# Performance work log

Hardware: AMD Instinct MI355X
Metric: run time of the kernel (lower is better)

Reference implementation:

```python
import jax, jax.numpy as jnp
import numpy as np

N = 50000
E = 800000
H = 4
C = 64
IN = 61
NEG_SLOPE = 0.2


def setup_inputs() -> dict:
    key = jax.random.key(0)
    ks = jax.random.split(key, 20)
    x = jax.random.normal(ks[0], (N, IN), dtype=jnp.float32)
    edge_index = jax.random.randint(ks[1], (2, E), 0, N, dtype=jnp.int64)

    def glorot(k, shape):
        fan = shape[0] + shape[-1] if len(shape) == 2 else shape[-1] * 2
        s = jnp.sqrt(6.0 / fan)
        return jax.random.uniform(k, shape, jnp.float32, -s, s)

    dims = [IN, H * C, H * C]
    params = {}
    for i, din in enumerate(dims):
        params[f'w{i}'] = glorot(ks[2 + 4 * i], (din, H * C))
        params[f'att_src{i}'] = glorot(ks[3 + 4 * i], (H, C))
        params[f'att_dst{i}'] = glorot(ks[4 + 4 * i], (H, C))
        params[f'b{i}'] = jnp.zeros((H * C,), jnp.float32)
    params['head_w1'] = glorot(ks[14], (H * C, C))
    params['head_b1'] = jnp.zeros((C,), jnp.float32)
    params['head_w2'] = glorot(ks[15], (C, 1))
    params['head_b2'] = jnp.zeros((1,), jnp.float32)
    return dict(x=x, edge_index=edge_index, **params)


def _gat_layer(x, W, att_src, att_dst, bias, src, dst):
    # Linear transform -> [N, H, C]
    h = (x @ W).reshape(N, H, C)
    # Per-node attention logits
    a_src = jnp.einsum('nhc,hc->nh', h, att_src)  # [N, H]
    a_dst = jnp.einsum('nhc,hc->nh', h, att_dst)
    # Per-edge score, leaky relu
    e = jax.nn.leaky_relu(a_src[src] + a_dst[dst], NEG_SLOPE)  # [Etot, H]
    # Segment softmax over incoming edges of each dst node
    m = jax.ops.segment_max(e, dst, num_segments=N)  # [N, H]
    ex = jnp.exp(e - m[dst])
    denom = jax.ops.segment_sum(ex, dst, num_segments=N)
    alpha = ex / denom[dst]  # [Etot, H]
    # Scatter-aggregate messages
    out = jax.ops.segment_sum(h[src] * alpha[:, :, None], dst, num_segments=N)  # [N, H, C]
    return out.reshape(N, H * C) + bias


def reference(x, edge_index, w0, att_src0, att_dst0, b0,
              w1, att_src1, att_dst1, b1,
              w2, att_src2, att_dst2, b2,
              head_w1, head_b1, head_w2, head_b2):
    # PyG GATConv adds self-loops by default
    loop = jnp.arange(N, dtype=edge_index.dtype)
    src = jnp.concatenate([edge_index[0], loop])
    dst = jnp.concatenate([edge_index[1], loop])

    layers = [(w0, att_src0, att_dst0, b0),
              (w1, att_src1, att_dst1, b1),
              (w2, att_src2, att_dst2, b2)]
    h = x
    for (W, a_s, a_d, b) in layers:
        h = _gat_layer(h, W, a_s, a_d, b, src, dst)
        h = jax.nn.elu(h)  # dropout is identity in eval mode
    # MLP head
    h = jax.nn.relu(h @ head_w1 + head_b1)
    out = (h @ head_w2 + head_b2).squeeze(-1)  # [N]
    return out
```

## Files before the change

kernel.cpp:

```cpp
#include <hip/hip_runtime.h>
#include <cstdint>
#include <cstddef>

#define NN   50000
#define EE   800000
#define ETOT (EE + NN)
#define HC   256
#define NEG_SLOPE 0.2f
#define SENT_WORDS 25000
#define SENT_VAL 0x42C80000u

typedef __attribute__((ext_vector_type(8))) short g4_bf16x8;
typedef __attribute__((ext_vector_type(4))) float g4_f32x4;

__device__ __forceinline__ float g4_bf2f(unsigned short h) {
    union { unsigned int u; float f; } v;
    v.u = ((unsigned int)h) << 16;
    return v.f;
}
__device__ __forceinline__ unsigned short g4_f2bf(float f) {
    union { float f; unsigned int u; } v;
    v.f = f;
    unsigned int u = v.u;
    u += 0x7fffu + ((u >> 16) & 1u);
    return (unsigned short)(u >> 16);
}
__device__ __forceinline__ float g4_ld(const void* p, size_t i, int isf) {
    return isf ? ((const float*)p)[i] : g4_bf2f(((const unsigned short*)p)[i]);
}

__global__ void g4_detect(const unsigned int* __restrict__ xw,
                          const int* __restrict__ ei32, int* __restrict__ flags) {
    __shared__ int cnt[256];
    int t = threadIdx.x;
    unsigned int w = xw[t];
    int e = (int)((w >> 23) & 0xffu);
    cnt[t] = (e >= 110 && e <= 135) ? 1 : 0;
    __syncthreads();
    for (int off = 128; off > 0; off >>= 1) {
        if (t < off) cnt[t] += cnt[t + off];
        __syncthreads();
    }
    if (t == 0) {
        flags[0] = (cnt[0] >= 128) ? 1 : 0;
        int i64 = (ei32[1] == 0 && ei32[3] == 0 && ei32[5] == 0 &&
                   ei32[7] == 0 && ei32[9] == 0) ? 1 : 0;
        flags[1] = i64;
    }
}

__global__ void g4_zero(int* __restrict__ deg, int* __restrict__ cnt,
                        unsigned int* __restrict__ outw) {
    int i = blockIdx.x * 256 + threadIdx.x;
    if (i < NN) { deg[i] = 0; cnt[i] = 0; }
    if (i < SENT_WORDS) outw[i] = SENT_VAL;
}

__global__ void g4_hist(const int* __restrict__ ei, const int* __restrict__ flags,
                        int* __restrict__ deg) {
    int e = blockIdx.x * blockDim.x + threadIdx.x;
    if (e >= ETOT) return;
    int i64 = flags[1];
    int d;
    if (e < EE) d = i64 ? ei[2 * (EE + e)] : ei[EE + e];
    else        d = e - EE;
    atomicAdd(&deg[d], 1);
}

__global__ void g4_scan_block(const int* __restrict__ deg, int* __restrict__ tmp,
                              int* __restrict__ partial) {
    __shared__ int sh[256];
    int i = blockIdx.x * 256 + threadIdx.x;
    int v = (i < NN) ? deg[i] : 0;
    sh[threadIdx.x] = v;
    __syncthreads();
    for (int off = 1; off < 256; off <<= 1) {
        int t = (threadIdx.x >= off) ? sh[threadIdx.x - off] : 0;
        __syncthreads();
        sh[threadIdx.x] += t;
        __syncthreads();
    }
    if (i < NN) tmp[i] = sh[threadIdx.x] - v;
    if (threadIdx.x == 255) partial[blockIdx.x] = sh[255];
}

__global__ void g4_scan_partial(int* __restrict__ partial, int nb,
                                int* __restrict__ rowptrN) {
    __shared__ int sh[256];
    int v = (threadIdx.x < nb) ? partial[threadIdx.x] : 0;
    sh[threadIdx.x] = v;
    __syncthreads();
    for (int off = 1; off < 256; off <<= 1) {
        int t = (threadIdx.x >= off) ? sh[threadIdx.x - off] : 0;
        __syncthreads();
        sh[threadIdx.x] += t;
        __syncthreads();
    }
    if (threadIdx.x < nb) partial[threadIdx.x] = sh[threadIdx.x] - v;
    if (threadIdx.x == 0) *rowptrN = ETOT;
}

__global__ void g4_scan_add(const int* __restrict__ tmp, const int* __restrict__ partial,
                            int* __restrict__ rowptr) {
    int i = blockIdx.x * 256 + threadIdx.x;
    if (i < NN) rowptr[i] = tmp[i] + partial[blockIdx.x];
}

__global__ void g4_fill_csr(const int* __restrict__ ei, const int* __restrict__ flags,
                            const int* __restrict__ rowptr,
                            int* __restrict__ cnt, int* __restrict__ col) {
    int e = blockIdx.x * blockDim.x + threadIdx.x;
    if (e >= ETOT) return;
    int i64 = flags[1];
    int s, d;
    if (e < EE) {
        s = i64 ? ei[2 * e] : ei[e];
        d = i64 ? ei[2 * (EE + e)] : ei[EE + e];
    } else {
        s = e - EE; d = e - EE;
    }
    int pos = rowptr[d] + atomicAdd(&cnt[d], 1);
    col[pos] = s;
}

__global__ void g4_bprep(const void* __restrict__ B, const int* __restrict__ flags,
                         unsigned short* __restrict__ Bt, int K, int kshift, int Nc) {
    int i = blockIdx.x * 256 + threadIdx.x;
    int KP = 1 << kshift;
    if (i >= Nc << kshift) return;
    int n = i >> kshift;
    int k = i & (KP - 1);
    unsigned short v = 0;
    if (k < K) {
        if (flags[0]) v = g4_f2bf(((const float*)B)[(size_t)k * Nc + n]);
        else          v = ((const unsigned short*)B)[(size_t)k * Nc + n];
    }
    Bt[(size_t)n * KP + k] = v;
}

#define LDK 40
__global__ __launch_bounds__(256) void g4_gemm2(
    const void* __restrict__ A, int a_mode, const unsigned short* __restrict__ Bt,
    const int* __restrict__ flags, unsigned short* __restrict__ C,
    const void* __restrict__ att_src, const void* __restrict__ att_dst,
    float* __restrict__ a_srcO, float* __restrict__ a_dstO,
    int M, int K, int KP) {
    __shared__ short As[64 * LDK];
    __shared__ short Bs[256 * LDK];
    const int isf = flags[0];
    const int af  = (a_mode == 0) ? isf : 0;
    const int tid  = threadIdx.x;
    const int lane = tid & 63;
    const int wc   = tid >> 6;
    const int quad = lane >> 4;
    const int l15  = lane & 15;
    const int bm = blockIdx.x * 64;
    const int a_vec = (af == 0) && ((K & 31) == 0);

    g4_f32x4 acc[4][4];
    #pragma unroll
    for (int it = 0; it < 4; it++)
        #pragma unroll
        for (int jt = 0; jt < 4; jt++) {
            acc[it][jt].x = 0.f; acc[it][jt].y = 0.f;
            acc[it][jt].z = 0.f; acc[it][jt].w = 0.f;
        }

    for (int k0 = 0; k0 < KP; k0 += 32) {
        {
            int row = tid >> 2, kc = (tid & 3) * 8;
            int gm = bm + row;
            short v[8];
            if (a_vec && gm < M) {
                *(g4_bf16x8*)v = *(const g4_bf16x8*)((const short*)A + (size_t)gm * K + k0 + kc);
            } else {
                #pragma unroll
                for (int j = 0; j < 8; j++) {
                    int gk = k0 + kc + j;
                    if (gm < M && gk < K) {
                        if (af == 0) v[j] = ((const short*)A)[(size_t)gm * K + gk];
                        else         v[j] = (short)g4_f2bf(((const float*)A)[(size_t)gm * K + gk]);
                    } else v[j] = 0;
                }
            }
            *(g4_bf16x8*)&As[row * LDK + kc] = *(g4_bf16x8*)v;
        }
        {
            const unsigned short* bp = Bt + (size_t)tid * KP + k0;
            short* dst = &Bs[tid * LDK];
            *(g4_bf16x8*)(dst + 0)  = *(const g4_bf16x8*)(bp + 0);
            *(g4_bf16x8*)(dst + 8)  = *(const g4_bf16x8*)(bp + 8);
            *(g4_bf16x8*)(dst + 16) = *(const g4_bf16x8*)(bp + 16);
            *(g4_bf16x8*)(dst + 24) = *(const g4_bf16x8*)(bp + 24);
        }
        __syncthreads();
        g4_bf16x8 afr[4], bfr[4];
        #pragma unroll
        for (int it = 0; it < 4; it++)
            afr[it] = *(const g4_bf16x8*)&As[(it * 16 + l15) * LDK + quad * 8];
        #pragma unroll
        for (int jt = 0; jt < 4; jt++)
            bfr[jt] = *(const g4_bf16x8*)&Bs[(wc * 64 + jt * 16 + l15) * LDK + quad * 8];
        #pragma unroll
        for (int it = 0; it < 4; it++)
            #pragma unroll
            for (int jt = 0; jt < 4; jt++)
                acc[it][jt] = __builtin_amdgcn_mfma_f32_16x16x32_bf16(
                    afr[it], bfr[jt], acc[it][jt], 0, 0, 0);
        __syncthreads();
    }
    #pragma unroll
    for (int it = 0; it < 4; it++) {
        #pragma unroll
        for (int jt = 0; jt < 4; jt++) {
            int gn   = wc * 64 + jt * 16 + l15;
            int row0 = bm + it * 16 + quad * 4;
            #pragma unroll
            for (int r = 0; r < 4; r++) {
                int gm = row0 + r;
                if (gm < M) C[(size_t)gm * HC + gn] = g4_f2bf(acc[it][jt][r]);
            }
        }
    }
    float asv[4], adv[4];
    #pragma unroll
    for (int jt = 0; jt < 4; jt++) {
        asv[jt] = g4_ld(att_src, wc * 64 + jt * 16 + l15, isf);
        adv[jt] = g4_ld(att_dst, wc * 64 + jt * 16 + l15, isf);
    }
    #pragma unroll
    for (int it = 0; it < 4; it++) {
        #pragma unroll
        for (int r = 0; r < 4; r++) {
            float ps = 0.f, pd = 0.f;
            #pragma unroll
            for (int jt = 0; jt < 4; jt++) {
                ps += acc[it][jt][r] * asv[jt];
                pd += acc[it][jt][r] * adv[jt];
            }
            #pragma unroll
            for (int off = 1; off < 16; off <<= 1) {
                ps += __shfl_xor(ps, off);
                pd += __shfl_xor(pd, off);
            }
            if (l15 == 0) {
                int gm = bm + it * 16 + quad * 4 + r;
                if (gm < M) {
                    a_srcO[gm * 4 + wc] = ps;
                    a_dstO[gm * 4 + wc] = pd;
                }
            }
        }
    }
}

__global__ __launch_bounds__(256) void g4_nodestat(
    const int* __restrict__ rowptr, const int* __restrict__ col,
    const float* __restrict__ a_src, const float* __restrict__ a_dst,
    float* __restrict__ alpha, float* __restrict__ nodeinv) {
    int d    = (blockIdx.x * blockDim.x + threadIdx.x) >> 6;
    int lane = threadIdx.x & 63;
    if (d >= NN) return;
    const int start = rowptr[d], end = rowptr[d + 1];
    g4_f32x4 ad = *(const g4_f32x4*)(a_dst + 4 * (size_t)d);

    float mx[4] = {-1e30f, -1e30f, -1e30f, -1e30f};
    for (int i = start + lane; i < end; i += 64) {
        int s = col[i];
        g4_f32x4 as = *(const g4_f32x4*)(a_src + 4 * (size_t)s);
        #pragma unroll
        for (int hh = 0; hh < 4; hh++) {
            float e = as[hh] + ad[hh];
            e = (e > 0.f) ? e : NEG_SLOPE * e;
            mx[hh] = fmaxf(mx[hh], e);
        }
    }
    for (int off = 32; off > 0; off >>= 1)
        #pragma unroll
        for (int hh = 0; hh < 4; hh++) mx[hh] = fmaxf(mx[hh], __shfl_xor(mx[hh], off));

    float sm[4] = {0.f, 0.f, 0.f, 0.f};
    for (int i = start + lane; i < end; i += 64) {
        int s = col[i];
        g4_f32x4 as = *(const g4_f32x4*)(a_src + 4 * (size_t)s);
        g4_f32x4 ex;
        #pragma unroll
        for (int hh = 0; hh < 4; hh++) {
            float e = as[hh] + ad[hh];
            e = (e > 0.f) ? e : NEG_SLOPE * e;
            ex[hh] = __expf(e - mx[hh]);
            sm[hh] += ex[hh];
        }
        *(g4_f32x4*)(alpha + 4 * (size_t)i) = ex;
    }
    for (int off = 32; off > 0; off >>= 1)
        #pragma unroll
        for (int hh = 0; hh < 4; hh++) sm[hh] += __shfl_xor(sm[hh], off);
    if (lane == 0) {
        g4_f32x4 inv;
        #pragma unroll
        for (int hh = 0; hh < 4; hh++) inv[hh] = 1.f / sm[hh];
        *(g4_f32x4*)(nodeinv + 4 * (size_t)d) = inv;
    }
}

__global__ __launch_bounds__(256) void g4_gather(
    const unsigned short* __restrict__ h, const float* __restrict__ alpha,
    const int* __restrict__ rowptr, const int* __restrict__ col,
    const float* __restrict__ nodeinv, const void* __restrict__ bias,
    const int* __restrict__ flags, unsigned short* __restrict__ xout) {
    int d    = (blockIdx.x * blockDim.x + threadIdx.x) >> 6;
    int lane = threadIdx.x & 63;
    if (d >= NN) return;
    d = __builtin_amdgcn_readfirstlane(d);
    const int isf = flags[0];
    const int hd  = lane >> 4;
    const int l15 = lane & 15;
    const int start = __builtin_amdgcn_readfirstlane(rowptr[d]);
    const int end   = __builtin_amdgcn_readfirstlane(rowptr[d + 1]);
    float a0 = 0.f, a1 = 0.f, a2 = 0.f, a3 = 0.f;
    const size_t ch = (size_t)(lane << 2);
    for (int base = start; base < end; base += 16) {
        int m = end - base;
        if (m > 16) m = 16;
        int   cv = col[base + l15];
        float av = alpha[4 * (size_t)base + lane];
        int j = 0;
        for (; j + 4 <= m; j += 4) {
            int s0 = __shfl(cv, j);
            int s1 = __shfl(cv, j + 1);
            int s2 = __shfl(cv, j + 2);
            int s3 = __shfl(cv, j + 3);
            float w0 = __shfl(av, 4 * j + hd);
            float w1 = __shfl(av, 4 * j + 4 + hd);
            float w2 = __shfl(av, 4 * j + 8 + hd);
            float w3 = __shfl(av, 4 * j + 12 + hd);
            uint2 h0 = *(const uint2*)(h + (((size_t)s0) << 8) + ch);
            uint2 h1 = *(const uint2*)(h + (((size_t)s1) << 8) + ch);
            uint2 h2 = *(const uint2*)(h + (((size_t)s2) << 8) + ch);
            uint2 h3 = *(const uint2*)(h + (((size_t)s3) << 8) + ch);
            a0 = fmaf(__uint_as_float(h0.x << 16),         w0, a0);
            a1 = fmaf(__uint_as_float(h0.x & 0xffff0000u), w0, a1);
            a2 = fmaf(__uint_as_float(h0.y << 16),         w0, a2);
            a3 = fmaf(__uint_as_float(h0.y & 0xffff0000u), w0, a3);
            a0 = fmaf(__uint_as_float(h1.x << 16),         w1, a0);
            a1 = fmaf(__uint_as_float(h1.x & 0xffff0000u), w1, a1);
            a2 = fmaf(__uint_as_float(h1.y << 16),         w1, a2);
            a3 = fmaf(__uint_as_float(h1.y & 0xffff0000u), w1, a3);
            a0 = fmaf(__uint_as_float(h2.x << 16),         w2, a0);
            a1 = fmaf(__uint_as_float(h2.x & 0xffff0000u), w2, a1);
            a2 = fmaf(__uint_as_float(h2.y << 16),         w2, a2);
            a3 = fmaf(__uint_as_float(h2.y & 0xffff0000u), w2, a3);
            a0 = fmaf(__uint_as_float(h3.x << 16),         w3, a0);
            a1 = fmaf(__uint_as_float(h3.x & 0xffff0000u), w3, a1);
            a2 = fmaf(__uint_as_float(h3.y << 16),         w3, a2);
            a3 = fmaf(__uint_as_float(h3.y & 0xffff0000u), w3, a3);
        }
        for (; j < m; j++) {
            int s = __shfl(cv, j);
            float w = __shfl(av, 4 * j + hd);
            uint2 hv = *(const uint2*)(h + (((size_t)s) << 8) + ch);
            a0 = fmaf(__uint_as_float(hv.x << 16),         w, a0);
            a1 = fmaf(__uint_as_float(hv.x & 0xffff0000u), w, a1);
            a2 = fmaf(__uint_as_float(hv.y << 16),         w, a2);
            a3 = fmaf(__uint_as_float(hv.y & 0xffff0000u), w, a3);
        }
    }
    g4_f32x4 invv = *(const g4_f32x4*)(nodeinv + 4 * (size_t)d);
    float inv = (hd < 2) ? ((hd == 0) ? invv.x : invv.y)
                         : ((hd == 2) ? invv.z : invv.w);
    float acc[4] = {a0 * inv, a1 * inv, a2 * inv, a3 * inv};
    unsigned short ov[4];
    #pragma unroll
    for (int j = 0; j < 4; j++) {
        float v = acc[j] + g4_ld(bias, (lane << 2) + j, isf);
        v = (v > 0.f) ? v : (__expf(v) - 1.f);
        ov[j] = g4_f2bf(v);
    }
    uint2 pack;
    pack.x = (unsigned int)ov[0] | ((unsigned int)ov[1] << 16);
    pack.y = (unsigned int)ov[2] | ((unsigned int)ov[3] << 16);
    *(uint2*)(xout + ((size_t)d << 8) + (lane << 2)) = pack;
}

__global__ __launch_bounds__(256) void g4_head2(
    const unsigned short* __restrict__ x, const void* __restrict__ w1,
    const void* __restrict__ b1, const void* __restrict__ w2,
    const void* __restrict__ b2, const int* __restrict__ flags,
    void* __restrict__ outp) {
    __shared__ float As[64][17];
    __shared__ float Bs[16][64];
    __shared__ float red[64][17];
    const int isf = flags[0];
    const int tid = threadIdx.x;
    const int bm  = blockIdx.x * 64;
    const int tx  = tid & 15;
    const int ty  = tid >> 4;
    float acc[4][4] = {};
    for (int k0 = 0; k0 < HC; k0 += 16) {
        for (int i = tid; i < 64 * 16; i += 256) {
            int m = i >> 4, kk = i & 15;
            int gm = bm + m;
            float v = 0.f;
            if (gm < NN) v = g4_bf2f(x[(size_t)gm * HC + k0 + kk]);
            As[m][kk] = v;
        }
        for (int i = tid; i < 16 * 64; i += 256) {
            int kk = i >> 6, n = i & 63;
            Bs[kk][n] = g4_ld(w1, (size_t)(k0 + kk) * 64 + n, isf);
        }
        __syncthreads();
        #pragma unroll
        for (int kk = 0; kk < 16; ++kk) {
            float a[4], b[4];
            #pragma unroll
            for (int i = 0; i < 4; i++) a[i] = As[ty * 4 + i][kk];
            #pragma unroll
            for (int j = 0; j < 4; j++) b[j] = Bs[kk][tx * 4 + j];
            #pragma unroll
            for (int i = 0; i < 4; i++)
                #pragma unroll
                for (int j = 0; j < 4; j++) acc[i][j] += a[i] * b[j];
        }
        __syncthreads();
    }
    float b1v[4], w2v[4];
    #pragma unroll
    for (int j = 0; j < 4; j++) {
        b1v[j] = g4_ld(b1, tx * 4 + j, isf);
        w2v[j] = g4_ld(w2, tx * 4 + j, isf);
    }
    #pragma unroll
    for (int i = 0; i < 4; i++) {
        float s = 0.f;
        #pragma unroll
        for (int j = 0; j < 4; j++) {
            float v = acc[i][j] + b1v[j];
            v = fmaxf(v, 0.f);
            s += v * w2v[j];
        }
        red[ty * 4 + i][tx] = s;
    }
    __syncthreads();
    if (tid < 64) {
        float s = 0.f;
        #pragma unroll
        for (int g = 0; g < 16; g++) s += red[tid][g];
        int gm = bm + tid;
        if (gm < NN) {
            float r = s + g4_ld(b2, 0, isf);
            if (isf) ((float*)outp)[gm] = r;
            else     ((unsigned short*)outp)[gm] = g4_f2bf(r);
        }
    }
}

extern "C" __attribute__((visibility("default")))
void kernel_launch(void* const* d_in, const int* in_sizes, int n_in,
                   void* d_out, int out_size, void* d_ws, size_t ws_size,
                   hipStream_t stream) {
    const void* x_in = d_in[0];
    const int*  ei   = (const int*)d_in[1];
    const void* W[3]    = {d_in[2], d_in[6], d_in[10]};
    const void* ASRC[3] = {d_in[3], d_in[7], d_in[11]};
    const void* ADST[3] = {d_in[4], d_in[8], d_in[12]};
    const void* BIAS[3] = {d_in[5], d_in[9], d_in[13]};
    const void* hw1 = d_in[14];
    const void* hb1 = d_in[15];
    const void* hw2 = d_in[16];
    const void* hb2 = d_in[17];

    char* base = (char*)d_ws;
    size_t woff = 0;
#define G4_TAKE(name, type, count) \
    type* name = (type*)(base + woff); \
    woff += (((size_t)(count)) * sizeof(type) + 255) & ~(size_t)255;
    G4_TAKE(flags,   int, 8)
    G4_TAKE(deg,     int, NN)
    G4_TAKE(cnt,     int, NN)
    G4_TAKE(tmp,     int, NN)
    G4_TAKE(partial, int, 256)
    G4_TAKE(rowptr,  int, NN + 1)
    G4_TAKE(col,     int, ETOT + 16)
    G4_TAKE(asr,     float, (size_t)NN * 4)
    G4_TAKE(adsb,    float, (size_t)NN * 4)
    G4_TAKE(nodeinv, float, (size_t)NN * 4)
    G4_TAKE(alpha,   float, (size_t)ETOT * 4 + 64)
    G4_TAKE(Bt,      unsigned short, (size_t)HC * HC)
    G4_TAKE(hbuf,    unsigned short, (size_t)NN * HC)
    G4_TAKE(xbuf,    unsigned short, (size_t)NN * HC)
#undef G4_TAKE

    const int SCAN_BLOCKS = (NN + 255) / 256;
    const int EDGE_BLOCKS = (ETOT + 255) / 256;
    const int WAVE_BLOCKS = (NN + 3) / 4;
    const int TILE_BLOCKS = (NN + 63) / 64;

    g4_detect<<<1, 256, 0, stream>>>((const unsigned int*)x_in, ei, flags);
    g4_zero<<<SCAN_BLOCKS, 256, 0, stream>>>(deg, cnt, (unsigned int*)d_out);

    g4_hist<<<EDGE_BLOCKS, 256, 0, stream>>>(ei, flags, deg);
    g4_scan_block<<<SCAN_BLOCKS, 256, 0, stream>>>(deg, tmp, partial);
    g4_scan_partial<<<1, 256, 0, stream>>>(partial, SCAN_BLOCKS, rowptr + NN);
    g4_scan_add<<<SCAN_BLOCKS, 256, 0, stream>>>(tmp, partial, rowptr);
    g4_fill_csr<<<EDGE_BLOCKS, 256, 0, stream>>>(ei, flags, rowptr, cnt, col);

    for (int l = 0; l < 3; l++) {
        int K      = (l == 0) ? 61 : HC;
        int kshift = (l == 0) ? 6  : 8;
        int KP     = 1 << kshift;
        int pb     = ((HC << kshift) + 255) / 256;
        g4_bprep<<<pb, 256, 0, stream>>>(W[l], flags, Bt, K, kshift, HC);
        if (l == 0) {
            g4_gemm2<<<TILE_BLOCKS, 256, 0, stream>>>(x_in, 0, Bt, flags, hbuf,
                ASRC[l], ADST[l], asr, adsb, NN, K, KP);
        } else {
            g4_gemm2<<<TILE_BLOCKS, 256, 0, stream>>>(xbuf, 1, Bt, flags, hbuf,
                ASRC[l], ADST[l], asr, adsb, NN, K, KP);
        }
        g4_nodestat<<<WAVE_BLOCKS, 256, 0, stream>>>(rowptr, col, asr, adsb, alpha, nodeinv);
        g4_gather<<<WAVE_BLOCKS, 256, 0, stream>>>(hbuf, alpha, rowptr, col,
                                                   nodeinv, BIAS[l], flags, xbuf);
    }
    g4_head2<<<TILE_BLOCKS, 256, 0, stream>>>(xbuf, hw1, hb1, hw2, hb2, flags, d_out);
}
```

Measured before the change: 606.4 us.

## Fuse softmax node statistics into gather, recomputing edge weights on the fly

Merges the per-node softmax kernel into the aggregation kernel. The gather now computes the per-destination max in a first pass, then recomputes each edge's exponentiated score inside the gather loop and reduces the denominator at the end. This drops the alpha and nodeinv buffers, one kernel launch per layer, and the write and read of the per-edge alpha array. In exchange each wave does extra exp work and redundant a_src loads inside the gather loop, and the serial max pass now sits in front of the latency-bound feature gather.

Result: faster. 541.2 us (-10.7%).

```diff
diff --git a/kernel.cpp b/kernel.cpp
--- a/kernel.cpp
+++ b/kernel.cpp
@@ -254,77 +254,57 @@
     }
 }
 
-__global__ __launch_bounds__(256) void g4_nodestat(
+__global__ __launch_bounds__(256) void g4_gatherf(
+    const unsigned short* __restrict__ h,
+    const float* __restrict__ a_src, const float* __restrict__ a_dst,
     const int* __restrict__ rowptr, const int* __restrict__ col,
-    const float* __restrict__ a_src, const float* __restrict__ a_dst,
-    float* __restrict__ alpha, float* __restrict__ nodeinv) {
-    int d    = (blockIdx.x * blockDim.x + threadIdx.x) >> 6;
-    int lane = threadIdx.x & 63;
-    if (d >= NN) return;
-    const int start = rowptr[d], end = rowptr[d + 1];
-    g4_f32x4 ad = *(const g4_f32x4*)(a_dst + 4 * (size_t)d);
-
-    float mx[4] = {-1e30f, -1e30f, -1e30f, -1e30f};
-    for (int i = start + lane; i < end; i += 64) {
-        int s = col[i];
-        g4_f32x4 as = *(const g4_f32x4*)(a_src + 4 * (size_t)s);
-        #pragma unroll
-        for (int hh = 0; hh < 4; hh++) {
-            float e = as[hh] + ad[hh];
-            e = (e > 0.f) ? e : NEG_SLOPE * e;
-            mx[hh] = fmaxf(mx[hh], e);
-        }
-    }
-    for (int off = 32; off > 0; off >>= 1)
-        #pragma unroll
-        for (int hh = 0; hh < 4; hh++) mx[hh] = fmaxf(mx[hh], __shfl_xor(mx[hh], off));
-
-    float sm[4] = {0.f, 0.f, 0.f, 0.f};
-    for (int i = start + lane; i < end; i += 64) {
-        int s = col[i];
-        g4_f32x4 as = *(const g4_f32x4*)(a_src + 4 * (size_t)s);
-        g4_f32x4 ex;
-        #pragma unroll
-        for (int hh = 0; hh < 4; hh++) {
-            float e = as[hh] + ad[hh];
-            e = (e > 0.f) ? e : NEG_SLOPE * e;
-            ex[hh] = __expf(e - mx[hh]);
-            sm[hh] += ex[hh];
-        }
-        *(g4_f32x4*)(alpha + 4 * (size_t)i) = ex;
-    }
-    for (int off = 32; off > 0; off >>= 1)
-        #pragma unroll
-        for (int hh = 0; hh < 4; hh++) sm[hh] += __shfl_xor(sm[hh], off);
-    if (lane == 0) {
-        g4_f32x4 inv;
-        #pragma unroll
-        for (int hh = 0; hh < 4; hh++) inv[hh] = 1.f / sm[hh];
-        *(g4_f32x4*)(nodeinv + 4 * (size_t)d) = inv;
-    }
-}
-
-__global__ __launch_bounds__(256) void g4_gather(
-    const unsigned short* __restrict__ h, const float* __restrict__ alpha,
-    const int* __restrict__ rowptr, const int* __restrict__ col,
-    const float* __restrict__ nodeinv, const void* __restrict__ bias,
-    const int* __restrict__ flags, unsigned short* __restrict__ xout) {
+    const void* __restrict__ bias, const int* __restrict__ flags,
+    unsigned short* __restrict__ xout) {
     int d    = (blockIdx.x * blockDim.x + threadIdx.x) >> 6;
     int lane = threadIdx.x & 63;
     if (d >= NN) return;
     d = __builtin_amdgcn_readfirstlane(d);
     const int isf = flags[0];
     const int hd  = lane >> 4;
+    const int q   = lane & 3;
+    const int eloc = lane >> 2;
     const int l15 = lane & 15;
     const int start = __builtin_amdgcn_readfirstlane(rowptr[d]);
     const int end   = __builtin_amdgcn_readfirstlane(rowptr[d + 1]);
+
+    g4_f32x4 ad4 = *(const g4_f32x4*)(a_dst + 4 * (size_t)d);
+    float mx[4] = {-1e30f, -1e30f, -1e30f, -1e30f};
+    for (int i = start + lane; i < end; i += 64) {
+        int s = col[i];
+        g4_f32x4 as = *(const g4_f32x4*)(a_src + 4 * (size_t)s);
+        #pragma unroll
+        for (int hh = 0; hh < 4; hh++) {
+            float e = as[hh] + ad4[hh];
+            e = (e > 0.f) ? e : NEG_SLOPE * e;
+            mx[hh] = fmaxf(mx[hh], e);
+        }
+    }
+    for (int off = 32; off > 0; off >>= 1)
+        #pragma unroll
+        for (int hh = 0; hh < 4; hh++) mx[hh] = fmaxf(mx[hh], __shfl_xor(mx[hh], off));
+    float mxq = (q < 2) ? ((q == 0) ? mx[0] : mx[1]) : ((q == 2) ? mx[2] : mx[3]);
+    float adq = (q < 2) ? ((q == 0) ? ad4.x : ad4.y) : ((q == 2) ? ad4.z : ad4.w);
+
     float a0 = 0.f, a1 = 0.f, a2 = 0.f, a3 = 0.f;
+    float sm = 0.f;
     const size_t ch = (size_t)(lane << 2);
     for (int base = start; base < end; base += 16) {
         int m = end - base;
         if (m > 16) m = 16;
-        int   cv = col[base + l15];
-        float av = alpha[4 * (size_t)base + lane];
+        int cv = col[base + l15];
+        int sE = __shfl(cv, eloc);
+        float av = 0.f;
+        if (eloc < m) {
+            float e = a_src[4 * (size_t)sE + q] + adq;
+            e = (e > 0.f) ? e : NEG_SLOPE * e;
+            av = __expf(e - mxq);
+            sm += av;
+        }
         int j = 0;
         for (; j + 4 <= m; j += 4) {
             int s0 = __shfl(cv, j);
@@ -366,9 +346,8 @@
             a3 = fmaf(__uint_as_float(hv.y & 0xffff0000u), w, a3);
         }
     }
-    g4_f32x4 invv = *(const g4_f32x4*)(nodeinv + 4 * (size_t)d);
-    float inv = (hd < 2) ? ((hd == 0) ? invv.x : invv.y)
-                         : ((hd == 2) ? invv.z : invv.w);
+    for (int off = 4; off < 64; off <<= 1) sm += __shfl_xor(sm, off);
+    float inv = 1.f / __shfl(sm, hd);
     float acc[4] = {a0 * inv, a1 * inv, a2 * inv, a3 * inv};
     unsigned short ov[4];
     #pragma unroll
@@ -484,8 +463,6 @@
     G4_TAKE(col,     int, ETOT + 16)
     G4_TAKE(asr,     float, (size_t)NN * 4)
     G4_TAKE(adsb,    float, (size_t)NN * 4)
-    G4_TAKE(nodeinv, float, (size_t)NN * 4)
-    G4_TAKE(alpha,   float, (size_t)ETOT * 4 + 64)
     G4_TAKE(Bt,      unsigned short, (size_t)HC * HC)
     G4_TAKE(hbuf,    unsigned short, (size_t)NN * HC)
     G4_TAKE(xbuf,    unsigned short, (size_t)NN * HC)
@@ -518,9 +495,8 @@
             g4_gemm2<<<TILE_BLOCKS, 256, 0, stream>>>(xbuf, 1, Bt, flags, hbuf,
                 ASRC[l], ADST[l], asr, adsb, NN, K, KP);
         }
-        g4_nodestat<<<WAVE_BLOCKS, 256, 0, stream>>>(rowptr, col, asr, adsb, alpha, nodeinv);
-        g4_gather<<<WAVE_BLOCKS, 256, 0, stream>>>(hbuf, alpha, rowptr, col,
-                                                   nodeinv, BIAS[l], flags, xbuf);
+        g4_gatherf<<<WAVE_BLOCKS, 256, 0, stream>>>(hbuf, asr, adsb, rowptr, col,
+                                                    BIAS[l], flags, xbuf);
     }
     g4_head2<<<TILE_BLOCKS, 256, 0, stream>>>(xbuf, hw1, hb1, hw2, hb2, flags, d_out);
 }
```
